# Kernel tuning notes

Measured on AMD Instinct MI355X. Metric: run time of the kernel, lower is better.

Reference implementation:

```python
import jax, jax.numpy as jnp
import numpy as np

N_HEAD, D_MODEL, D_K, D_V = 16, 1024, 64, 64
B, L = 8, 1024
LN_EPS = 1e-5
NEG_INF = -1e9


def setup_inputs() -> dict:
    key = jax.random.key(0)
    ks = jax.random.split(key, 12)
    s = 0.02
    return {
        "q": jax.random.normal(ks[0], (B, L, D_MODEL), jnp.float32),
        "k": jax.random.normal(ks[1], (B, L, D_MODEL), jnp.float32),
        "v": jax.random.normal(ks[2], (B, L, D_MODEL), jnp.float32),
        "mask": jnp.zeros((B, L, L), dtype=bool),
        "wq": jax.random.normal(ks[3], (D_MODEL, N_HEAD * D_K), jnp.float32) * s,
        "bq": jnp.zeros((N_HEAD * D_K,), jnp.float32),
        "wk": jax.random.normal(ks[4], (D_MODEL, N_HEAD * D_K), jnp.float32) * s,
        "bk": jnp.zeros((N_HEAD * D_K,), jnp.float32),
        "wv": jax.random.normal(ks[5], (D_MODEL, N_HEAD * D_V), jnp.float32) * s,
        "bv": jnp.zeros((N_HEAD * D_V,), jnp.float32),
        "wo": jax.random.normal(ks[6], (N_HEAD * D_V, D_MODEL), jnp.float32) * s,
        "bo": jnp.zeros((D_MODEL,), jnp.float32),
        "gamma": jnp.ones((D_MODEL,), jnp.float32),
        "beta": jnp.zeros((D_MODEL,), jnp.float32),
    }


def reference(q, k, v, mask, wq, bq, wk, bk, wv, bv, wo, bo, gamma, beta):
    b, lq, _ = q.shape
    lk = k.shape[1]
    residual = q
    # separate Q/K/V projections, split heads: [b, len, h, d]
    qh = (q @ wq + bq).reshape(b, lq, N_HEAD, D_K)
    kh = (k @ wk + bk).reshape(b, lk, N_HEAD, D_K)
    vh = (v @ wv + bv).reshape(b, lk, N_HEAD, D_V)
    # scaled dot-product attention (temperature = sqrt(d_k))
    scores = jnp.einsum("bqhd,bkhd->bhqk", qh, kh) / jnp.sqrt(jnp.float32(D_K))
    scores = jnp.where(mask[:, None, :, :], NEG_INF, scores)
    attn = jax.nn.softmax(scores, axis=-1)  # [b, h, lq, lk]
    ctx = jnp.einsum("bhqk,bkhd->bqhd", attn, vh).reshape(b, lq, N_HEAD * D_V)
    # out-proj (dropout is identity in eval) + residual + LayerNorm
    out = ctx @ wo + bo + residual
    mu = out.mean(-1, keepdims=True)
    var = out.var(-1, keepdims=True)
    out = (out - mu) * jax.lax.rsqrt(var + LN_EPS) * gamma + beta
    # match original attn layout: [n_head*b, lq, lk]
    attn_flat = attn.transpose(1, 0, 2, 3).reshape(N_HEAD * b, lq, lk)
    return out, attn_flat
```

## Files before the change

### kernel.cpp

```cpp
#include <hip/hip_runtime.h>
#include <stdint.h>

static constexpr int BATCH  = 8;
static constexpr int SEQ    = 1024;
static constexpr int DMODEL = 1024;
static constexpr int NHEAD  = 16;

typedef __attribute__((ext_vector_type(8))) short sh8;
typedef __attribute__((ext_vector_type(4))) float fl4;

__device__ __forceinline__ uint16_t f2bf(float f) {
    union { float f; uint32_t u; } a; a.f = f;
    uint32_t r = a.u + 0x7FFFu + ((a.u >> 16) & 1u);
    return (uint16_t)(r >> 16);
}

__device__ __forceinline__ float b2f(uint16_t u) {
    union { uint32_t u; float f; } a; a.u = ((uint32_t)u) << 16; return a.f;
}

__device__ __forceinline__ uint32_t cvtpk(float lo, float hi) {
    uint32_t r;
    asm("v_cvt_pk_bf16_f32 %0, %1, %2" : "=v"(r) : "v"(lo), "v"(hi));
    return r;
}

__device__ __forceinline__ sh8 pack_bf8(fl4 x0, fl4 x1) {
    union { uint32_t w[4]; sh8 v; } pk;
    pk.w[0] = cvtpk(x0[0], x0[1]); pk.w[1] = cvtpk(x0[2], x0[3]);
    pk.w[2] = cvtpk(x1[0], x1[1]); pk.w[3] = cvtpk(x1[2], x1[3]);
    return pk.v;
}

__device__ __forceinline__ fl4 mfma16(sh8 a, sh8 b, fl4 c) {
    return __builtin_amdgcn_mfma_f32_16x16x32_bf16(a, b, c, 0, 0, 0);
}

__device__ __forceinline__ void gload16(const void* g, void* l) {
    __builtin_amdgcn_global_load_lds(
        (const __attribute__((address_space(1))) void*)g,
        (__attribute__((address_space(3))) void*)l, 16, 0, 0);
}

__global__ __launch_bounds__(256) void prep_kernel(const float* __restrict__ wq, const float* __restrict__ wk,
                                                   const float* __restrict__ wv, const float* __restrict__ wo,
                                                   uint16_t* __restrict__ tq, uint16_t* __restrict__ tk,
                                                   uint16_t* __restrict__ tv, uint16_t* __restrict__ to,
                                                   const float* __restrict__ q, const float* __restrict__ k,
                                                   const float* __restrict__ v,
                                                   uint16_t* __restrict__ dq, uint16_t* __restrict__ dk,
                                                   uint16_t* __restrict__ dv) {
    __shared__ uint16_t T[64][72];
    const int z = blockIdx.z;
    const int tid = threadIdx.x;
    if (z < 4) {
        const float* w = (z == 0) ? wq : (z == 1) ? wk : (z == 2) ? wv : wo;
        uint16_t* wT = (z == 0) ? tq : (z == 1) ? tk : (z == 2) ? tv : to;
        const float ws = (z == 0) ? 0.125f : 1.f;
        const int n0 = blockIdx.x * 64, k0 = blockIdx.y * 64;
        #pragma unroll
        for (int it = 0; it < 4; ++it) {
            int g = it * 256 + tid;
            int r = g >> 4, c = (g & 15) * 4;
            fl4 x = *(const fl4*)(w + (size_t)(k0 + r) * DMODEL + n0 + c);
            T[r][c + 0] = f2bf(x[0] * ws); T[r][c + 1] = f2bf(x[1] * ws);
            T[r][c + 2] = f2bf(x[2] * ws); T[r][c + 3] = f2bf(x[3] * ws);
        }
        __syncthreads();
        #pragma unroll
        for (int it = 0; it < 4; ++it) {
            int g = it * 256 + tid;
            int r = g >> 4, c = (g & 15) * 4;
            ushort4 o;
            o.x = T[c + 0][r]; o.y = T[c + 1][r]; o.z = T[c + 2][r]; o.w = T[c + 3][r];
            *(ushort4*)(wT + (size_t)(n0 + r) * DMODEL + k0 + c) = o;
        }
    } else {
        const int zz = z - 4;
        const float* src = (zz == 0) ? q : (zz == 1) ? k : v;
        uint16_t* dst = (zz == 0) ? dq : (zz == 1) ? dk : dv;
        const int bid = blockIdx.y * 16 + blockIdx.x;
        #pragma unroll
        for (int it = 0; it < 16; ++it) {
            const size_t i = ((size_t)bid * 4096 + it * 256 + tid) * 8;
            fl4 x0 = *(const fl4*)(src + i), x1 = *(const fl4*)(src + i + 4);
            *(sh8*)(dst + i) = pack_bf8(x0, x1);
        }
    }
}

__global__ __launch_bounds__(256) void vtrans_kernel(const uint16_t* __restrict__ vh,
                                                     uint16_t* __restrict__ vT) {
    __shared__ uint16_t T[64][72];
    const int l0 = blockIdx.x * 64, hd0 = blockIdx.y * 64, bb = blockIdx.z;
    const uint16_t* src = vh + (size_t)bb * SEQ * DMODEL;
    uint16_t* dst = vT + (size_t)bb * SEQ * DMODEL;
    const int tid = threadIdx.x;
    #pragma unroll
    for (int it = 0; it < 4; ++it) {
        int g = it * 256 + tid;
        int r = g >> 4, c = (g & 15) * 4;
        ushort4 x = *(const ushort4*)(src + (size_t)(l0 + r) * DMODEL + hd0 + c);
        T[r][c + 0] = x.x; T[r][c + 1] = x.y; T[r][c + 2] = x.z; T[r][c + 3] = x.w;
    }
    __syncthreads();
    #pragma unroll
    for (int it = 0; it < 4; ++it) {
        int g = it * 256 + tid;
        int r = g >> 4, c = (g & 15) * 4;
        ushort4 o;
        o.x = T[c + 0][r]; o.y = T[c + 1][r]; o.z = T[c + 2][r]; o.w = T[c + 3][r];
        *(ushort4*)(dst + (size_t)(hd0 + r) * DMODEL + l0 + c) = o;
    }
}

template<bool OUT_BF16, bool RESID>
__device__ __forceinline__
void gemm_body(const uint16_t* __restrict__ Ab, const uint16_t* __restrict__ Bt,
               const float* __restrict__ bias, float bscale, const float* __restrict__ resid,
               void* __restrict__ Cv, int m0, int n0, uint16_t* lds) {
    uint16_t* Alds = lds;
    uint16_t* Blds = lds + 128 * 64;
    const int tid = threadIdx.x;
    const int lane = tid & 63, wid = tid >> 6;
    const int wr = (wid >> 1) * 64, wc = (wid & 1) * 64;
    const int fr = lane & 15, fk = (lane >> 4) * 8, frow4 = (lane >> 4) * 4;

    fl4 acc[4][4];
    #pragma unroll
    for (int i = 0; i < 4; ++i)
        #pragma unroll
        for (int j = 0; j < 4; ++j) acc[i][j] = (fl4){0.f, 0.f, 0.f, 0.f};

    for (int kt = 0; kt < 16; ++kt) {
        const int kb = kt * 64;
        #pragma unroll
        for (int it = 0; it < 4; ++it) {
            const int g = it * 256 + tid;
            const int r = g >> 3, c = (g & 7) << 3;
            const int lofs = __builtin_amdgcn_readfirstlane((it * 256 + wid * 64) * 16);
            gload16(Ab + (size_t)(m0 + r) * DMODEL + kb + c, (char*)Alds + lofs);
            gload16(Bt + (size_t)(n0 + r) * DMODEL + kb + c, (char*)Blds + lofs);
        }
        __syncthreads();
        #pragma unroll
        for (int ks = 0; ks < 2; ++ks) {
            sh8 a[4], bb[4];
            #pragma unroll
            for (int mi = 0; mi < 4; ++mi) a[mi] = *(const sh8*)&Alds[(wr + mi * 16 + fr) * 64 + ks * 32 + fk];
            #pragma unroll
            for (int ni = 0; ni < 4; ++ni) bb[ni] = *(const sh8*)&Blds[(wc + ni * 16 + fr) * 64 + ks * 32 + fk];
            #pragma unroll
            for (int mi = 0; mi < 4; ++mi)
                #pragma unroll
                for (int ni = 0; ni < 4; ++ni) acc[mi][ni] = mfma16(a[mi], bb[ni], acc[mi][ni]);
        }
        __syncthreads();
    }

    if (OUT_BF16) {
        #pragma unroll
        for (int mi = 0; mi < 4; ++mi) {
            #pragma unroll
            for (int ni = 0; ni < 4; ++ni) {
                const int col = wc + ni * 16 + fr;
                const float bv = bias[n0 + col] * bscale;
                #pragma unroll
                for (int i = 0; i < 4; ++i) {
                    const int row = wr + mi * 16 + frow4 + i;
                    lds[row * 128 + ((((col >> 3) ^ (row & 7)) << 3) | (col & 7))] = f2bf(acc[mi][ni][i] + bv);
                }
            }
        }
        __syncthreads();
        #pragma unroll
        for (int it = 0; it < 8; ++it) {
            const int ch = it * 256 + tid;
            const int row = ch >> 4, cc = ch & 15;
            sh8 vv = *(sh8*)&lds[row * 128 + ((cc ^ (row & 7)) << 3)];
            *(sh8*)((uint16_t*)Cv + (size_t)(m0 + row) * DMODEL + n0 + cc * 8) = vv;
        }
    } else {
        float* flds = (float*)lds;
        #pragma unroll
        for (int h2 = 0; h2 < 2; ++h2) {
            if (h2) __syncthreads();
            if (wc == h2 * 64) {
                #pragma unroll
                for (int ni = 0; ni < 4; ++ni) {
                    const int col = wc + ni * 16 + fr;
                    const int ch = col - h2 * 64;
                    const float bv = bias[n0 + col] * bscale;
                    #pragma unroll
                    for (int i = 0; i < 4; ++i) {
                        const int row = wr + (0) * 16 + frow4 + i; (void)row;
                    }
                    #pragma unroll
                    for (int mi = 0; mi < 4; ++mi) {
                        #pragma unroll
                        for (int i = 0; i < 4; ++i) {
                            const int row = wr + mi * 16 + frow4 + i;
                            float val = acc[mi][ni][i] + bv;
                            if (RESID) val += resid[(size_t)(m0 + row) * DMODEL + n0 + col];
                            flds[row * 64 + ((((ch >> 2) ^ (row & 7)) << 2) | (ch & 3))] = val;
                        }
                    }
                }
            }
            __syncthreads();
            #pragma unroll
            for (int it = 0; it < 8; ++it) {
                const int ck = it * 256 + tid;
                const int row = ck >> 4, cc = ck & 15;
                fl4 vv = *(fl4*)&flds[row * 64 + ((cc ^ (row & 7)) << 2)];
                *(fl4*)((float*)Cv + (size_t)(m0 + row) * DMODEL + n0 + h2 * 64 + cc * 4) = vv;
            }
        }
    }
}

__global__ __launch_bounds__(256)
void gemm_proj(const uint16_t* __restrict__ A0, const uint16_t* __restrict__ A1, const uint16_t* __restrict__ A2,
               const uint16_t* __restrict__ B0, const uint16_t* __restrict__ B1, const uint16_t* __restrict__ B2,
               const float* __restrict__ b0, const float* __restrict__ b1, const float* __restrict__ b2,
               uint16_t* __restrict__ C0, uint16_t* __restrict__ C1, uint16_t* __restrict__ C2) {
    __shared__ uint16_t lds[2 * 128 * 64];
    const int z = blockIdx.z;
    const uint16_t* Ab = (z == 0) ? A0 : (z == 1) ? A1 : A2;
    const uint16_t* Bt = (z == 0) ? B0 : (z == 1) ? B1 : B2;
    const float* bias  = (z == 0) ? b0 : (z == 1) ? b1 : b2;
    uint16_t* Cv       = (z == 0) ? C0 : (z == 1) ? C1 : C2;
    const float bs     = (z == 0) ? 0.125f : 1.f;
    gemm_body<true, false>(Ab, Bt, bias, bs, nullptr, Cv, blockIdx.x * 128, blockIdx.y * 128, lds);
}

__global__ __launch_bounds__(256)
void gemm_out(const uint16_t* __restrict__ Ab, const uint16_t* __restrict__ Bt,
              const float* __restrict__ bias, const float* __restrict__ resid,
              float* __restrict__ Cv) {
    __shared__ uint16_t lds[2 * 128 * 64];
    gemm_body<false, true>(Ab, Bt, bias, 1.f, resid, Cv, blockIdx.x * 128, blockIdx.y * 128, lds);
}

__global__ __launch_bounds__(256)
void attn_kernel(const uint16_t* __restrict__ qh, const uint16_t* __restrict__ kh,
                 const uint16_t* __restrict__ vT, const uint8_t* __restrict__ mask,
                 float* __restrict__ attn, uint16_t* __restrict__ ctx) {
    __shared__ uint16_t S[16 * 1024];
    __shared__ float rinv[16];
    const int b = blockIdx.x, h = blockIdx.y, q0 = blockIdx.z * 16;
    const int tid = threadIdx.x, lane = tid & 63, wid = tid >> 6;
    const int fr = lane & 15, fk = (lane >> 4) * 8, frow4 = (lane >> 4) * 4;

    sh8 Aq[2];
    #pragma unroll
    for (int ks = 0; ks < 2; ++ks)
        Aq[ks] = *(const sh8*)(qh + (size_t)(b * SEQ + q0 + fr) * DMODEL + h * 64 + ks * 32 + fk);

    for (int t8 = 0; t8 < 8; ++t8) {
        const int kv0 = (t8 * 4 + wid) * 32;
        sh8 Bk[2][2];
        #pragma unroll
        for (int ni = 0; ni < 2; ++ni)
            #pragma unroll
            for (int ks = 0; ks < 2; ++ks)
                Bk[ni][ks] = *(const sh8*)(kh + (size_t)(b * SEQ + kv0 + ni * 16 + fr) * DMODEL + h * 64 + ks * 32 + fk);
        fl4 sa[2];
        #pragma unroll
        for (int ni = 0; ni < 2; ++ni) sa[ni] = (fl4){0.f, 0.f, 0.f, 0.f};
        #pragma unroll
        for (int ni = 0; ni < 2; ++ni)
            #pragma unroll
            for (int ks = 0; ks < 2; ++ks) sa[ni] = mfma16(Aq[ks], Bk[ni][ks], sa[ni]);
        #pragma unroll
        for (int ni = 0; ni < 2; ++ni)
            #pragma unroll
            for (int i = 0; i < 4; ++i) {
                const int row = frow4 + i, col = kv0 + ni * 16 + fr;
                S[row * 1024 + ((((col >> 3) ^ (row & 15)) << 3) | (col & 7))] = f2bf(sa[ni][i]);
            }
    }
    __syncthreads();

    {
        const int r = tid >> 4, j = tid & 15;
        const int rbase = r * 1024;
        const uint8_t* mbase = mask + (size_t)(b * SEQ + q0 + r) * SEQ;
        sh8 x[8];
        uint2 mw[8];
        float mx = -1e30f;
        #pragma unroll
        for (int c4 = 0; c4 < 8; ++c4) {
            const int cc = c4 * 16 + j;
            x[c4] = *(sh8*)&S[rbase + ((cc ^ r) << 3)];
            mw[c4] = *(const uint2*)(mbase + cc * 8);
            #pragma unroll
            for (int t = 0; t < 4; ++t) {
                float f = ((mw[c4].x >> (t * 8)) & 0xFF) ? -1e9f : b2f((uint16_t)x[c4][t]);
                mx = fmaxf(mx, f);
            }
            #pragma unroll
            for (int t = 0; t < 4; ++t) {
                float f = ((mw[c4].y >> (t * 8)) & 0xFF) ? -1e9f : b2f((uint16_t)x[c4][4 + t]);
                mx = fmaxf(mx, f);
            }
        }
        #pragma unroll
        for (int d = 1; d < 16; d <<= 1) mx = fmaxf(mx, __shfl_xor(mx, d));
        float sum = 0.f;
        #pragma unroll
        for (int c4 = 0; c4 < 8; ++c4) {
            const int cc = c4 * 16 + j;
            float e[8];
            #pragma unroll
            for (int t = 0; t < 4; ++t) {
                float f = ((mw[c4].x >> (t * 8)) & 0xFF) ? -1e9f : b2f((uint16_t)x[c4][t]);
                e[t] = __expf(f - mx);
            }
            #pragma unroll
            for (int t = 0; t < 4; ++t) {
                float f = ((mw[c4].y >> (t * 8)) & 0xFF) ? -1e9f : b2f((uint16_t)x[c4][4 + t]);
                e[4 + t] = __expf(f - mx);
            }
            union { uint32_t w[4]; sh8 v; } pk;
            pk.w[0] = cvtpk(e[0], e[1]); pk.w[1] = cvtpk(e[2], e[3]);
            pk.w[2] = cvtpk(e[4], e[5]); pk.w[3] = cvtpk(e[6], e[7]);
            *(sh8*)&S[rbase + ((cc ^ r) << 3)] = pk.v;
            sum += e[0] + e[1] + e[2] + e[3] + e[4] + e[5] + e[6] + e[7];
        }
        #pragma unroll
        for (int d = 1; d < 16; d <<= 1) sum += __shfl_xor(sum, d);
        if (j == 0) rinv[r] = 1.f / sum;
    }
    __syncthreads();

    fl4 acc0 = (fl4){0.f, 0.f, 0.f, 0.f}, acc1 = (fl4){0.f, 0.f, 0.f, 0.f};
    const uint16_t* vbase = vT + (size_t)((b * NHEAD + h) * 64 + wid * 16) * SEQ;
    #pragma unroll 4
    for (int ks2 = 0; ks2 < 32; ++ks2) {
        const int kv = ks2 * 32;
        sh8 Ap = *(const sh8*)&S[fr * 1024 + ((((kv + fk) >> 3) ^ fr) << 3)];
        sh8 Bv = *(const sh8*)(vbase + (size_t)fr * SEQ + kv + fk);
        if (ks2 & 1) acc1 = mfma16(Ap, Bv, acc1);
        else         acc0 = mfma16(Ap, Bv, acc0);
    }
    #pragma unroll
    for (int i = 0; i < 4; ++i) {
        const int q = frow4 + i;
        const float val = (acc0[i] + acc1[i]) * rinv[q];
        ctx[(size_t)(b * SEQ + q0 + q) * DMODEL + h * 64 + wid * 16 + fr] = f2bf(val);
    }

    {
        float* ab = attn + ((size_t)((h * BATCH + b) * SEQ + q0)) * SEQ;
        #pragma unroll
        for (int it = 0; it < 16; ++it) {
            const int ch = it * 256 + tid;
            const int row = ch >> 8, oc = ch & 255;
            const int cc = oc >> 1, half = oc & 1;
            const ushort4 p = *(const ushort4*)&S[row * 1024 + ((cc ^ row) << 3) + half * 4];
            const float ri = rinv[row];
            fl4 o;
            o[0] = b2f(p.x) * ri; o[1] = b2f(p.y) * ri;
            o[2] = b2f(p.z) * ri; o[3] = b2f(p.w) * ri;
            __builtin_nontemporal_store(o, (fl4*)(ab + (size_t)ch * 4));
        }
    }
}

__global__ __launch_bounds__(256)
void ln_kernel(const float* __restrict__ raw, const float* __restrict__ gamma,
               const float* __restrict__ beta, float* __restrict__ out) {
    const int row = blockIdx.x;
    const int tid = threadIdx.x;
    const float* x = raw + (size_t)row * DMODEL;
    fl4 xv = *(const fl4*)(x + tid * 4);
    float s  = xv[0] + xv[1] + xv[2] + xv[3];
    float ss = xv[0] * xv[0] + xv[1] * xv[1] + xv[2] * xv[2] + xv[3] * xv[3];
    #pragma unroll
    for (int d = 1; d < 64; d <<= 1) { s += __shfl_xor(s, d); ss += __shfl_xor(ss, d); }
    __shared__ float sb[4], ssb[4];
    if ((tid & 63) == 0) { sb[tid >> 6] = s; ssb[tid >> 6] = ss; }
    __syncthreads();
    s  = sb[0] + sb[1] + sb[2] + sb[3];
    ss = ssb[0] + ssb[1] + ssb[2] + ssb[3];
    const float mu  = s * (1.f / 1024.f);
    const float var = ss * (1.f / 1024.f) - mu * mu;
    const float rstd = rsqrtf(var + 1e-5f);
    fl4 g  = *(const fl4*)(gamma + tid * 4);
    fl4 be = *(const fl4*)(beta + tid * 4);
    fl4 o;
    #pragma unroll
    for (int j = 0; j < 4; ++j) o[j] = (xv[j] - mu) * rstd * g[j] + be[j];
    *(fl4*)(out + (size_t)row * DMODEL + tid * 4) = o;
}

extern "C" void kernel_launch(void* const* d_in, const int* in_sizes, int n_in,
                              void* d_out, int out_size, void* d_ws, size_t ws_size,
                              hipStream_t stream) {
    (void)in_sizes; (void)n_in; (void)out_size; (void)ws_size;
    const float* q     = (const float*)d_in[0];
    const float* k     = (const float*)d_in[1];
    const float* v     = (const float*)d_in[2];
    const uint8_t* mask = (const uint8_t*)d_in[3];
    const float* wq = (const float*)d_in[4];
    const float* bq = (const float*)d_in[5];
    const float* wk = (const float*)d_in[6];
    const float* bk = (const float*)d_in[7];
    const float* wv = (const float*)d_in[8];
    const float* bv = (const float*)d_in[9];
    const float* wo = (const float*)d_in[10];
    const float* bo = (const float*)d_in[11];
    const float* gamma = (const float*)d_in[12];
    const float* beta  = (const float*)d_in[13];

    float* out  = (float*)d_out;
    float* attn = out + (size_t)BATCH * SEQ * DMODEL;

    uint16_t* qcvt = (uint16_t*)(attn);
    uint16_t* kcvt = (uint16_t*)((char*)attn + ((size_t)16 << 20));
    uint16_t* vcvt = (uint16_t*)((char*)attn + ((size_t)32 << 20));

    char* ws = (char*)d_ws;
    uint16_t* qh   = (uint16_t*)(ws);
    uint16_t* kh   = (uint16_t*)(ws + ((size_t)16 << 20));
    uint16_t* vT   = (uint16_t*)(ws + ((size_t)32 << 20));
    uint16_t* ctx  = (uint16_t*)(ws + ((size_t)48 << 20));
    uint16_t* wqT  = (uint16_t*)(ws + ((size_t)64 << 20));
    uint16_t* wkT  = (uint16_t*)(ws + ((size_t)66 << 20));
    uint16_t* wvT  = (uint16_t*)(ws + ((size_t)68 << 20));
    uint16_t* woT  = (uint16_t*)(ws + ((size_t)70 << 20));
    uint16_t* vtmp = (uint16_t*)(ws + ((size_t)72 << 20));

    dim3 tb(256);
    prep_kernel<<<dim3(16, 16, 7), tb, 0, stream>>>(wq, wk, wv, wo, wqT, wkT, wvT, woT,
                                                    q, k, v, qcvt, kcvt, vcvt);

    gemm_proj<<<dim3(64, 8, 3), tb, 0, stream>>>(qcvt, kcvt, vcvt, wqT, wkT, wvT,
                                                 bq, bk, bv, qh, kh, vtmp);

    vtrans_kernel<<<dim3(16, 16, 8), tb, 0, stream>>>(vtmp, vT);

    attn_kernel<<<dim3(BATCH, NHEAD, 64), tb, 0, stream>>>(qh, kh, vT, mask, attn, ctx);

    gemm_out<<<dim3(64, 8), tb, 0, stream>>>(ctx, woT, bo, q, out);

    ln_kernel<<<BATCH * SEQ, tb, 0, stream>>>(out, gamma, beta, out);
}
```

Before: 449.1 us.

## Fuse fp32-to-bf16 input conversion and V transpose into projection GEMM

The projection GEMM now reads fp32 q/k/v directly and converts them to bf16 while staging into LDS, which removes the separate conversion pass and its bf16 round-trip through memory. The V projection writes its output transposed through LDS, so the standalone vtrans kernel is gone. In the attention kernel the P·V product now runs after the attn-probability store, and ctx is written through LDS as coalesced rows. In exchange, A-tile loads become synchronous register loads instead of async global-to-LDS copies, which could expose memory latency in the GEMM main loop.

```diff
diff --git a/kernel.cpp b/kernel.cpp
--- a/kernel.cpp
+++ b/kernel.cpp
@@ -45,63 +45,21 @@
 __global__ __launch_bounds__(256) void prep_kernel(const float* __restrict__ wq, const float* __restrict__ wk,
                                                    const float* __restrict__ wv, const float* __restrict__ wo,
                                                    uint16_t* __restrict__ tq, uint16_t* __restrict__ tk,
-                                                   uint16_t* __restrict__ tv, uint16_t* __restrict__ to,
-                                                   const float* __restrict__ q, const float* __restrict__ k,
-                                                   const float* __restrict__ v,
-                                                   uint16_t* __restrict__ dq, uint16_t* __restrict__ dk,
-                                                   uint16_t* __restrict__ dv) {
+                                                   uint16_t* __restrict__ tv, uint16_t* __restrict__ to) {
     __shared__ uint16_t T[64][72];
     const int z = blockIdx.z;
     const int tid = threadIdx.x;
-    if (z < 4) {
-        const float* w = (z == 0) ? wq : (z == 1) ? wk : (z == 2) ? wv : wo;
-        uint16_t* wT = (z == 0) ? tq : (z == 1) ? tk : (z == 2) ? tv : to;
-        const float ws = (z == 0) ? 0.125f : 1.f;
-        const int n0 = blockIdx.x * 64, k0 = blockIdx.y * 64;
-        #pragma unroll
-        for (int it = 0; it < 4; ++it) {
-            int g = it * 256 + tid;
-            int r = g >> 4, c = (g & 15) * 4;
-            fl4 x = *(const fl4*)(w + (size_t)(k0 + r) * DMODEL + n0 + c);
-            T[r][c + 0] = f2bf(x[0] * ws); T[r][c + 1] = f2bf(x[1] * ws);
-            T[r][c + 2] = f2bf(x[2] * ws); T[r][c + 3] = f2bf(x[3] * ws);
-        }
-        __syncthreads();
-        #pragma unroll
-        for (int it = 0; it < 4; ++it) {
-            int g = it * 256 + tid;
-            int r = g >> 4, c = (g & 15) * 4;
-            ushort4 o;
-            o.x = T[c + 0][r]; o.y = T[c + 1][r]; o.z = T[c + 2][r]; o.w = T[c + 3][r];
-            *(ushort4*)(wT + (size_t)(n0 + r) * DMODEL + k0 + c) = o;
-        }
-    } else {
-        const int zz = z - 4;
-        const float* src = (zz == 0) ? q : (zz == 1) ? k : v;
-        uint16_t* dst = (zz == 0) ? dq : (zz == 1) ? dk : dv;
-        const int bid = blockIdx.y * 16 + blockIdx.x;
-        #pragma unroll
-        for (int it = 0; it < 16; ++it) {
-            const size_t i = ((size_t)bid * 4096 + it * 256 + tid) * 8;
-            fl4 x0 = *(const fl4*)(src + i), x1 = *(const fl4*)(src + i + 4);
-            *(sh8*)(dst + i) = pack_bf8(x0, x1);
-        }
-    }
-}
-
-__global__ __launch_bounds__(256) void vtrans_kernel(const uint16_t* __restrict__ vh,
-                                                     uint16_t* __restrict__ vT) {
-    __shared__ uint16_t T[64][72];
-    const int l0 = blockIdx.x * 64, hd0 = blockIdx.y * 64, bb = blockIdx.z;
-    const uint16_t* src = vh + (size_t)bb * SEQ * DMODEL;
-    uint16_t* dst = vT + (size_t)bb * SEQ * DMODEL;
-    const int tid = threadIdx.x;
+    const float* w = (z == 0) ? wq : (z == 1) ? wk : (z == 2) ? wv : wo;
+    uint16_t* wT = (z == 0) ? tq : (z == 1) ? tk : (z == 2) ? tv : to;
+    const float ws = (z == 0) ? 0.125f : 1.f;
+    const int n0 = blockIdx.x * 64, k0 = blockIdx.y * 64;
     #pragma unroll
     for (int it = 0; it < 4; ++it) {
         int g = it * 256 + tid;
         int r = g >> 4, c = (g & 15) * 4;
-        ushort4 x = *(const ushort4*)(src + (size_t)(l0 + r) * DMODEL + hd0 + c);
-        T[r][c + 0] = x.x; T[r][c + 1] = x.y; T[r][c + 2] = x.z; T[r][c + 3] = x.w;
+        fl4 x = *(const fl4*)(w + (size_t)(k0 + r) * DMODEL + n0 + c);
+        T[r][c + 0] = f2bf(x[0] * ws); T[r][c + 1] = f2bf(x[1] * ws);
+        T[r][c + 2] = f2bf(x[2] * ws); T[r][c + 3] = f2bf(x[3] * ws);
     }
     __syncthreads();
     #pragma unroll
@@ -110,19 +68,120 @@
         int r = g >> 4, c = (g & 15) * 4;
         ushort4 o;
         o.x = T[c + 0][r]; o.y = T[c + 1][r]; o.z = T[c + 2][r]; o.w = T[c + 3][r];
-        *(ushort4*)(dst + (size_t)(hd0 + r) * DMODEL + l0 + c) = o;
-    }
-}
-
-template<bool OUT_BF16, bool RESID>
-__device__ __forceinline__
-void gemm_body(const uint16_t* __restrict__ Ab, const uint16_t* __restrict__ Bt,
-               const float* __restrict__ bias, float bscale, const float* __restrict__ resid,
-               void* __restrict__ Cv, int m0, int n0, uint16_t* lds) {
+        *(ushort4*)(wT + (size_t)(n0 + r) * DMODEL + k0 + c) = o;
+    }
+}
+
+__global__ __launch_bounds__(256)
+void gemm_proj(const float* __restrict__ q, const float* __restrict__ k, const float* __restrict__ v,
+               const uint16_t* __restrict__ B0, const uint16_t* __restrict__ B1, const uint16_t* __restrict__ B2,
+               const float* __restrict__ b0, const float* __restrict__ b1, const float* __restrict__ b2,
+               uint16_t* __restrict__ qh, uint16_t* __restrict__ kh, uint16_t* __restrict__ vT) {
+    __shared__ uint16_t lds[128 * 128];
     uint16_t* Alds = lds;
     uint16_t* Blds = lds + 128 * 64;
-    const int tid = threadIdx.x;
-    const int lane = tid & 63, wid = tid >> 6;
+    const int z = blockIdx.z;
+    const float* Af    = (z == 0) ? q : (z == 1) ? k : v;
+    const uint16_t* Bt = (z == 0) ? B0 : (z == 1) ? B1 : B2;
+    const float* bias  = (z == 0) ? b0 : (z == 1) ? b1 : b2;
+    const float bs     = (z == 0) ? 0.125f : 1.f;
+    const int m0 = blockIdx.x * 128, n0 = blockIdx.y * 128;
+    const int tid = threadIdx.x, lane = tid & 63, wid = tid >> 6;
+    const int wr = (wid >> 1) * 64, wc = (wid & 1) * 64;
+    const int fr = lane & 15, fk = (lane >> 4) * 8, frow4 = (lane >> 4) * 4;
+
+    fl4 acc[4][4];
+    #pragma unroll
+    for (int i = 0; i < 4; ++i)
+        #pragma unroll
+        for (int j = 0; j < 4; ++j) acc[i][j] = (fl4){0.f, 0.f, 0.f, 0.f};
+
+    for (int kt = 0; kt < 16; ++kt) {
+        const int kb = kt * 64;
+        #pragma unroll
+        for (int it = 0; it < 4; ++it) {
+            const int g = it * 256 + tid;
+            const int r = g >> 3, c = (g & 7) << 3;
+            const float* p = Af + (size_t)(m0 + r) * DMODEL + kb + c;
+            fl4 x0 = *(const fl4*)p, x1 = *(const fl4*)(p + 4);
+            *(sh8*)&Alds[r * 64 + c] = pack_bf8(x0, x1);
+            const int lofs = __builtin_amdgcn_readfirstlane((it * 256 + wid * 64) * 16);
+            gload16(Bt + (size_t)(n0 + r) * DMODEL + kb + c, (char*)Blds + lofs);
+        }
+        __syncthreads();
+        #pragma unroll
+        for (int ks = 0; ks < 2; ++ks) {
+            sh8 a[4], bb[4];
+            #pragma unroll
+            for (int mi = 0; mi < 4; ++mi) a[mi] = *(const sh8*)&Alds[(wr + mi * 16 + fr) * 64 + ks * 32 + fk];
+            #pragma unroll
+            for (int ni = 0; ni < 4; ++ni) bb[ni] = *(const sh8*)&Blds[(wc + ni * 16 + fr) * 64 + ks * 32 + fk];
+            #pragma unroll
+            for (int mi = 0; mi < 4; ++mi)
+                #pragma unroll
+                for (int ni = 0; ni < 4; ++ni) acc[mi][ni] = mfma16(a[mi], bb[ni], acc[mi][ni]);
+        }
+        __syncthreads();
+    }
+
+    if (z < 2) {
+        #pragma unroll
+        for (int mi = 0; mi < 4; ++mi) {
+            #pragma unroll
+            for (int ni = 0; ni < 4; ++ni) {
+                const int col = wc + ni * 16 + fr;
+                const float bv = bias[n0 + col] * bs;
+                #pragma unroll
+                for (int i = 0; i < 4; ++i) {
+                    const int row = wr + mi * 16 + frow4 + i;
+                    lds[row * 128 + ((((col >> 3) ^ (row & 7)) << 3) | (col & 7))] = f2bf(acc[mi][ni][i] + bv);
+                }
+            }
+        }
+        __syncthreads();
+        uint16_t* Cv = (z == 0) ? qh : kh;
+        #pragma unroll
+        for (int it = 0; it < 8; ++it) {
+            const int ch = it * 256 + tid;
+            const int row = ch >> 4, cc = ch & 15;
+            sh8 vv = *(sh8*)&lds[row * 128 + ((cc ^ (row & 7)) << 3)];
+            *(sh8*)(Cv + (size_t)(m0 + row) * DMODEL + n0 + cc * 8) = vv;
+        }
+    } else {
+        #pragma unroll
+        for (int mi = 0; mi < 4; ++mi) {
+            #pragma unroll
+            for (int ni = 0; ni < 4; ++ni) {
+                const int col = wc + ni * 16 + fr;
+                const float bv = bias[n0 + col];
+                #pragma unroll
+                for (int i = 0; i < 4; ++i) {
+                    const int row = wr + mi * 16 + frow4 + i;
+                    lds[col * 128 + ((((row >> 3) ^ (col & 7)) << 3) | (row & 7))] = f2bf(acc[mi][ni][i] + bv);
+                }
+            }
+        }
+        __syncthreads();
+        const int b = m0 >> 10, l0 = m0 & 1023;
+        #pragma unroll
+        for (int it = 0; it < 8; ++it) {
+            const int ch = it * 256 + tid;
+            const int col = ch >> 4, rc = ch & 15;
+            sh8 vv = *(sh8*)&lds[col * 128 + ((rc ^ (col & 7)) << 3)];
+            *(sh8*)(vT + (size_t)(b * 1024 + n0 + col) * SEQ + l0 + rc * 8) = vv;
+        }
+    }
+}
+
+__global__ __launch_bounds__(256)
+void gemm_out(const uint16_t* __restrict__ Ab, const uint16_t* __restrict__ Bt,
+              const float* __restrict__ bias, const float* __restrict__ resid,
+              float* __restrict__ Cv) {
+    __shared__ uint16_t lds[128 * 128];
+    uint16_t* Alds = lds;
+    uint16_t* Blds = lds + 128 * 64;
+    const int m0 = blockIdx.x * 128, n0 = blockIdx.y * 128;
+    const int tid = threadIdx.x, lane = tid & 63, wid = tid >> 6;
     const int wr = (wid >> 1) * 64, wc = (wid & 1) * 64;
     const int fr = lane & 15, fk = (lane >> 4) * 8, frow4 = (lane >> 4) * 4;
 
@@ -158,88 +217,37 @@
         __syncthreads();
     }
 
-    if (OUT_BF16) {
-        #pragma unroll
-        for (int mi = 0; mi < 4; ++mi) {
+    float* flds = (float*)lds;
+    #pragma unroll
+    for (int h2 = 0; h2 < 2; ++h2) {
+        if (h2) __syncthreads();
+        if (wc == h2 * 64) {
             #pragma unroll
             for (int ni = 0; ni < 4; ++ni) {
                 const int col = wc + ni * 16 + fr;
-                const float bv = bias[n0 + col] * bscale;
+                const int ch = col - h2 * 64;
+                const float bv = bias[n0 + col];
                 #pragma unroll
-                for (int i = 0; i < 4; ++i) {
-                    const int row = wr + mi * 16 + frow4 + i;
-                    lds[row * 128 + ((((col >> 3) ^ (row & 7)) << 3) | (col & 7))] = f2bf(acc[mi][ni][i] + bv);
-                }
-            }
-        }
-        __syncthreads();
-        #pragma unroll
-        for (int it = 0; it < 8; ++it) {
-            const int ch = it * 256 + tid;
-            const int row = ch >> 4, cc = ch & 15;
-            sh8 vv = *(sh8*)&lds[row * 128 + ((cc ^ (row & 7)) << 3)];
-            *(sh8*)((uint16_t*)Cv + (size_t)(m0 + row) * DMODEL + n0 + cc * 8) = vv;
-        }
-    } else {
-        float* flds = (float*)lds;
-        #pragma unroll
-        for (int h2 = 0; h2 < 2; ++h2) {
-            if (h2) __syncthreads();
-            if (wc == h2 * 64) {
-                #pragma unroll
-                for (int ni = 0; ni < 4; ++ni) {
-                    const int col = wc + ni * 16 + fr;
-                    const int ch = col - h2 * 64;
-                    const float bv = bias[n0 + col] * bscale;
+                for (int mi = 0; mi < 4; ++mi) {
                     #pragma unroll
                     for (int i = 0; i < 4; ++i) {
-                        const int row = wr + (0) * 16 + frow4 + i; (void)row;
-                    }
-                    #pragma unroll
-                    for (int mi = 0; mi < 4; ++mi) {
-                        #pragma unroll
-                        for (int i = 0; i < 4; ++i) {
-                            const int row = wr + mi * 16 + frow4 + i;
-                            float val = acc[mi][ni][i] + bv;
-                            if (RESID) val += resid[(size_t)(m0 + row) * DMODEL + n0 + col];
-                            flds[row * 64 + ((((ch >> 2) ^ (row & 7)) << 2) | (ch & 3))] = val;
-                        }
+                        const int row = wr + mi * 16 + frow4 + i;
+                        float val = acc[mi][ni][i] + bv;
+                        val += resid[(size_t)(m0 + row) * DMODEL + n0 + col];
+                        flds[row * 64 + ((((ch >> 2) ^ (row & 7)) << 2) | (ch & 3))] = val;
                     }
                 }
             }
-            __syncthreads();
-            #pragma unroll
-            for (int it = 0; it < 8; ++it) {
-                const int ck = it * 256 + tid;
-                const int row = ck >> 4, cc = ck & 15;
-                fl4 vv = *(fl4*)&flds[row * 64 + ((cc ^ (row & 7)) << 2)];
-                *(fl4*)((float*)Cv + (size_t)(m0 + row) * DMODEL + n0 + h2 * 64 + cc * 4) = vv;
-            }
-        }
-    }
-}
-
-__global__ __launch_bounds__(256)
-void gemm_proj(const uint16_t* __restrict__ A0, const uint16_t* __restrict__ A1, const uint16_t* __restrict__ A2,
-               const uint16_t* __restrict__ B0, const uint16_t* __restrict__ B1, const uint16_t* __restrict__ B2,
-               const float* __restrict__ b0, const float* __restrict__ b1, const float* __restrict__ b2,
-               uint16_t* __restrict__ C0, uint16_t* __restrict__ C1, uint16_t* __restrict__ C2) {
-    __shared__ uint16_t lds[2 * 128 * 64];
-    const int z = blockIdx.z;
-    const uint16_t* Ab = (z == 0) ? A0 : (z == 1) ? A1 : A2;
-    const uint16_t* Bt = (z == 0) ? B0 : (z == 1) ? B1 : B2;
-    const float* bias  = (z == 0) ? b0 : (z == 1) ? b1 : b2;
-    uint16_t* Cv       = (z == 0) ? C0 : (z == 1) ? C1 : C2;
-    const float bs     = (z == 0) ? 0.125f : 1.f;
-    gemm_body<true, false>(Ab, Bt, bias, bs, nullptr, Cv, blockIdx.x * 128, blockIdx.y * 128, lds);
-}
-
-__global__ __launch_bounds__(256)
-void gemm_out(const uint16_t* __restrict__ Ab, const uint16_t* __restrict__ Bt,
-              const float* __restrict__ bias, const float* __restrict__ resid,
-              float* __restrict__ Cv) {
-    __shared__ uint16_t lds[2 * 128 * 64];
-    gemm_body<false, true>(Ab, Bt, bias, 1.f, resid, Cv, blockIdx.x * 128, blockIdx.y * 128, lds);
+        }
+        __syncthreads();
+        #pragma unroll
+        for (int it = 0; it < 8; ++it) {
+            const int ck = it * 256 + tid;
+            const int row = ck >> 4, cc = ck & 15;
+            fl4 vv = *(fl4*)&flds[row * 64 + ((cc ^ (row & 7)) << 2)];
+            *(fl4*)(Cv + (size_t)(m0 + row) * DMODEL + n0 + h2 * 64 + cc * 4) = vv;
+        }
+    }
 }
 
 __global__ __launch_bounds__(256)
@@ -333,23 +341,6 @@
         if (j == 0) rinv[r] = 1.f / sum;
     }
     __syncthreads();
-
-    fl4 acc0 = (fl4){0.f, 0.f, 0.f, 0.f}, acc1 = (fl4){0.f, 0.f, 0.f, 0.f};
-    const uint16_t* vbase = vT + (size_t)((b * NHEAD + h) * 64 + wid * 16) * SEQ;
-    #pragma unroll 4
-    for (int ks2 = 0; ks2 < 32; ++ks2) {
-        const int kv = ks2 * 32;
-        sh8 Ap = *(const sh8*)&S[fr * 1024 + ((((kv + fk) >> 3) ^ fr) << 3)];
-        sh8 Bv = *(const sh8*)(vbase + (size_t)fr * SEQ + kv + fk);
-        if (ks2 & 1) acc1 = mfma16(Ap, Bv, acc1);
-        else         acc0 = mfma16(Ap, Bv, acc0);
-    }
-    #pragma unroll
-    for (int i = 0; i < 4; ++i) {
-        const int q = frow4 + i;
-        const float val = (acc0[i] + acc1[i]) * rinv[q];
-        ctx[(size_t)(b * SEQ + q0 + q) * DMODEL + h * 64 + wid * 16 + fr] = f2bf(val);
-    }
 
     {
         float* ab = attn + ((size_t)((h * BATCH + b) * SEQ + q0)) * SEQ;
@@ -365,6 +356,31 @@
             o[2] = b2f(p.z) * ri; o[3] = b2f(p.w) * ri;
             __builtin_nontemporal_store(o, (fl4*)(ab + (size_t)ch * 4));
         }
+    }
+
+    fl4 acc0 = (fl4){0.f, 0.f, 0.f, 0.f}, acc1 = (fl4){0.f, 0.f, 0.f, 0.f};
+    const uint16_t* vbase = vT + (size_t)((b * NHEAD + h) * 64 + wid * 16) * SEQ;
+    #pragma unroll 4
+    for (int ks2 = 0; ks2 < 32; ++ks2) {
+        const int kv = ks2 * 32;
+        sh8 Ap = *(const sh8*)&S[fr * 1024 + ((((kv + fk) >> 3) ^ fr) << 3)];
+        sh8 Bv = *(const sh8*)(vbase + (size_t)fr * SEQ + kv + fk);
+        if (ks2 & 1) acc1 = mfma16(Ap, Bv, acc1);
+        else         acc0 = mfma16(Ap, Bv, acc0);
+    }
+    __syncthreads();
+
+    {
+        uint16_t* Sc = S;
+        #pragma unroll
+        for (int i = 0; i < 4; ++i) {
+            const int qr = frow4 + i;
+            Sc[qr * 64 + wid * 16 + fr] = f2bf((acc0[i] + acc1[i]) * rinv[qr]);
+        }
+        __syncthreads();
+        const int row = tid >> 4, c4 = (tid & 15) * 4;
+        ushort4 vv = *(ushort4*)&Sc[row * 64 + c4];
+        *(ushort4*)(ctx + (size_t)(b * SEQ + q0 + row) * DMODEL + h * 64 + c4) = vv;
     }
 }
 
@@ -417,10 +433,6 @@
     float* out  = (float*)d_out;
     float* attn = out + (size_t)BATCH * SEQ * DMODEL;
 
-    uint16_t* qcvt = (uint16_t*)(attn);
-    uint16_t* kcvt = (uint16_t*)((char*)attn + ((size_t)16 << 20));
-    uint16_t* vcvt = (uint16_t*)((char*)attn + ((size_t)32 << 20));
-
     char* ws = (char*)d_ws;
     uint16_t* qh   = (uint16_t*)(ws);
     uint16_t* kh   = (uint16_t*)(ws + ((size_t)16 << 20));
@@ -430,16 +442,12 @@
     uint16_t* wkT  = (uint16_t*)(ws + ((size_t)66 << 20));
     uint16_t* wvT  = (uint16_t*)(ws + ((size_t)68 << 20));
     uint16_t* woT  = (uint16_t*)(ws + ((size_t)70 << 20));
-    uint16_t* vtmp = (uint16_t*)(ws + ((size_t)72 << 20));
 
     dim3 tb(256);
-    prep_kernel<<<dim3(16, 16, 7), tb, 0, stream>>>(wq, wk, wv, wo, wqT, wkT, wvT, woT,
-                                                    q, k, v, qcvt, kcvt, vcvt);
-
-    gemm_proj<<<dim3(64, 8, 3), tb, 0, stream>>>(qcvt, kcvt, vcvt, wqT, wkT, wvT,
-                                                 bq, bk, bv, qh, kh, vtmp);
-
-    vtrans_kernel<<<dim3(16, 16, 8), tb, 0, stream>>>(vtmp, vT);
+    prep_kernel<<<dim3(16, 16, 4), tb, 0, stream>>>(wq, wk, wv, wo, wqT, wkT, wvT, woT);
+
+    gemm_proj<<<dim3(64, 8, 3), tb, 0, stream>>>(q, k, v, wqT, wkT, wvT,
+                                                 bq, bk, bv, qh, kh, vT);
 
     attn_kernel<<<dim3(BATCH, NHEAD, 64), tb, 0, stream>>>(qh, kh, vT, mask, attn, ctx);
 
```

New measurement: 415.3 us. 7.5% less time.
